# Kernel optimization log

Hardware: AMD Instinct MI355X
Metric: run time of the kernel (lower is better)

Reference implementation:

```python
import jax, jax.numpy as jnp
import numpy as np

T, K = 131072, 128  # turns, num_tags


def setup_inputs() -> dict:
    key = jax.random.key(0)
    ks = jax.random.split(key, 8)
    emissions = jax.random.normal(ks[0], (T, K), dtype=jnp.float32)
    tags = jax.random.randint(ks[1], (T,), 0, K)
    who2who = jax.random.randint(ks[2], (T - 1,), 0, 2)
    init_count = jax.random.randint(ks[3], (T - 1,), 0, 2)
    distance = jax.random.randint(ks[4], (T - 1,), 0, 3)
    class_weights = jax.random.uniform(ks[5], (K,), jnp.float32, 0.5, 1.5)
    # DistanceCRF transition matrices stacked: [s2u, u2s_n0, u2s_n1_d2, u2s_n1_dgt2]
    trans_stack = jax.random.normal(ks[6], (4, K, K), dtype=jnp.float32) * 0.1
    start_scores = jax.random.normal(ks[7], (K,), dtype=jnp.float32) * 0.1
    return {
        "emissions": emissions,
        "trans_stack": trans_stack,
        "start_scores": start_scores,
        "class_weights": class_weights,
        "tags": tags,
        "who2who": who2who,
        "init_count": init_count,
        "distance": distance,
    }


def _trans_idx(who2who, init_count, distance):
    # DistanceCRF decision tree from _get_trans:
    #   w==1 -> s2u (0); init_count==0 -> u2s_n0 (1);
    #   distance==0 -> u2s_n1_d2 (2); else -> u2s_n1_dgt2 (3)
    return jnp.where(
        who2who == 1, 0,
        jnp.where(init_count == 0, 1, jnp.where(distance == 0, 2, 3)),
    )


def reference(emissions, trans_stack, start_scores, class_weights,
              tags, who2who, init_count, distance):
    idx = _trans_idx(who2who, init_count, distance)  # [T-1]

    # ---- gold path score (fully vectorized) ----
    w = class_weights[tags]                                   # [T]
    em_gold = jnp.take_along_axis(emissions, tags[:, None], axis=1)[:, 0]  # [T]
    tr_gold = trans_stack[idx, tags[:-1], tags[1:]]           # [T-1]
    gold = w[0] * (start_scores[tags[0]] + em_gold[0]) \
        + jnp.sum(w[1:] * (tr_gold + em_gold[1:]))

    # ---- forward algorithm (log partition) ----
    def step(alphas, xs):
        i, em_t = xs
        tr = trans_stack[i]                                   # [K,K] gathered per step
        scores = alphas[:, None] + tr + em_t[None, :]         # [K,K]
        return jax.nn.logsumexp(scores, axis=0), None

    alpha0 = start_scores + emissions[0]
    alphas, _ = jax.lax.scan(step, alpha0, (idx, emissions[1:]))
    log_Z = jax.nn.logsumexp(alphas)
    return gold, log_Z
```

## Files before the change

### kernel.cpp

```cpp
#include <hip/hip_runtime.h>

#define T_LEN 131072
#define KDIM 128
#define CHUNK 16
#define WARM 16
#define NSTEP (CHUNK + WARM)
#define NCHUNK (T_LEN / CHUNK)
#define GROUPC 16
#define NGRP (NCHUNK / GROUPC)
#define CSHIFT 4.5f

typedef float v4f __attribute__((ext_vector_type(4)));
typedef short s8v __attribute__((ext_vector_type(8)));

__device__ __forceinline__ int trans_idx(int w2w, int ic, int dist) {
    return (w2w == 1) ? 0 : (ic == 0 ? 1 : (dist == 0 ? 2 : 3));
}
__device__ __forceinline__ unsigned short bf16rne(float x) {
    unsigned u = __float_as_uint(x);
    return (unsigned short)((u + 0x7fffu + ((u >> 16) & 1u)) >> 16);
}
__device__ __forceinline__ float bf16tof(unsigned short h) {
    return __uint_as_float(((unsigned)h) << 16);
}

__global__ void __launch_bounds__(256) scan_kernel(
    const float* __restrict__ em, const float* __restrict__ trans,
    const float* __restrict__ start, const float* __restrict__ cw,
    const int* __restrict__ tags, const int* __restrict__ w2w,
    const int* __restrict__ ic, const int* __restrict__ dist,
    double* __restrict__ goldslots, double* __restrict__ logzslots,
    unsigned* __restrict__ donecnt, float* __restrict__ out)
{
    const int tid = threadIdx.x;
    const int wv  = tid >> 6;
    const int ln  = tid & 63;
    const int lr  = ln & 15;
    const int hq  = ln >> 4;
    const int grp = blockIdx.x;

    __shared__ float SS[32][130];
    __shared__ __align__(16) unsigned short A[2][GROUPC * KDIM];
    __shared__ double bg[4];
    __shared__ double bzred[4];
    __shared__ double redd[256];
    __shared__ int islast;

    s8v Bf[4][2][4];
    const int ncol = (wv << 5) + lr;
    {
        const int sr = tid >> 3;
        const int sc = (tid & 7) << 4;
        float4 nx0, nx1, nx2, nx3;
        {
            const float* s = trans + (tid << 4);
            nx0 = *(const float4*)(s);     nx1 = *(const float4*)(s + 4);
            nx2 = *(const float4*)(s + 8); nx3 = *(const float4*)(s + 12);
        }
        #pragma unroll
        for (int p = 0; p < 16; ++p) {
            const int m = p >> 2, ks = p & 3;
            ((float2*)&SS[sr][sc])[0] = make_float2(nx0.x, nx0.y);
            ((float2*)&SS[sr][sc])[1] = make_float2(nx0.z, nx0.w);
            ((float2*)&SS[sr][sc + 4])[0] = make_float2(nx1.x, nx1.y);
            ((float2*)&SS[sr][sc + 4])[1] = make_float2(nx1.z, nx1.w);
            ((float2*)&SS[sr][sc + 8])[0] = make_float2(nx2.x, nx2.y);
            ((float2*)&SS[sr][sc + 8])[1] = make_float2(nx2.z, nx2.w);
            ((float2*)&SS[sr][sc + 12])[0] = make_float2(nx3.x, nx3.y);
            ((float2*)&SS[sr][sc + 12])[1] = make_float2(nx3.z, nx3.w);
            __syncthreads();
            if (p < 15) {
                const float* s = trans + ((p + 1) << 12) + (tid << 4);
                nx0 = *(const float4*)(s);     nx1 = *(const float4*)(s + 4);
                nx2 = *(const float4*)(s + 8); nx3 = *(const float4*)(s + 12);
            }
            s8v f0, f1;
            #pragma unroll
            for (int j = 0; j < 8; ++j) {
                f0[j] = (short)bf16rne(__expf(SS[(hq << 3) + j][ncol]));
                f1[j] = (short)bf16rne(__expf(SS[(hq << 3) + j][ncol + 16]));
            }
            Bf[m][0][ks] = f0;
            Bf[m][1][ks] = f1;
            __syncthreads();
        }
    }

    {
        float gp = 0.f;
        const int t = 1 + (grp << 8) + tid;
        if (t < T_LEN) {
            const int tg  = tags[t];
            const int tgp = tags[t - 1];
            const int mm  = trans_idx(w2w[t - 1], ic[t - 1], dist[t - 1]);
            gp = cw[tg] * (trans[((size_t)mm * KDIM + tgp) * KDIM + tg] +
                           em[(size_t)t * KDIM + tg]);
        }
        if (grp == 0 && tid == 0) {
            const int tg0 = tags[0];
            gp += cw[tg0] * (start[tg0] + em[tg0]);
        }
        float r = gp;
        #pragma unroll
        for (int off = 32; off; off >>= 1) r += __shfl_down(r, off, 64);
        if (ln == 0) bg[wv] = (double)r;
    }

    if (wv == 0) {
        const int c_row = (grp << 4) + lr;
        #pragma unroll
        for (int kk = 0; kk < 32; kk += 2) {
            const int k = (hq << 5) + kk;
            float a0, a1;
            if (c_row == 0) {
                a0 = __expf(start[k] + em[k]);
                a1 = __expf(start[k + 1] + em[k + 1]);
            } else { a0 = 1.f; a1 = 1.f; }
            const int off = (lr << 8) + ((k << 1) ^ ((lr & 7) << 4));
            *(unsigned*)((char*)A[0] + off) =
                (unsigned)bf16rne(a0) | ((unsigned)bf16rne(a1) << 16);
        }
    }
    __syncthreads();

    int t0r[4];
    #pragma unroll
    for (int r = 0; r < 4; ++r) {
        const int c_r = (grp << 4) + (hq << 2) + r;
        t0r[r] = (c_r == 0) ? 1 : (1 + c_r * CHUNK - WARM);
    }
    const int c_lr   = (grp << 4) + lr;
    const int town_l = 1 + c_lr * CHUNK;
    const int tend_l = min(town_l + CHUNK, T_LEN);
    const int t0_l   = (c_lr == 0) ? 1 : (town_l - WARM);

    int pmw, pmi, pmd;
    {
        const int ix = min(t0_l - 1, T_LEN - 2);
        pmw = w2w[ix]; pmi = ic[ix]; pmd = dist[ix];
    }
    float pem[2][4];
    #pragma unroll
    for (int r = 0; r < 4; ++r) {
        const int t = min(t0r[r], T_LEN - 1);
        pem[0][r] = em[(size_t)t * KDIM + ncol];
        pem[1][r] = em[(size_t)t * KDIM + ncol + 16];
    }

    float g = 0.f;
    float sc4[4] = {1.f, 1.f, 1.f, 1.f};

    for (int it = 0; it <= NSTEP; ++it) {
        s8v Af[4];
        #pragma unroll
        for (int ks = 0; ks < 4; ++ks) {
            const int off = (lr << 8) + (((ks << 6) + (hq << 4)) ^ ((lr & 7) << 4));
            Af[ks] = *(const s8v*)((const char*)A[it & 1] + off);
        }

        const bool trig = ((it & 7) == 0) || (grp == NGRP - 1 && it == NSTEP - 1);
        if (trig) {
            float s = 0.f;
            #pragma unroll
            for (int ks = 0; ks < 4; ++ks) {
                #pragma unroll
                for (int j = 0; j < 8; ++j)
                    s += bf16tof((unsigned short)Af[ks][j]);
            }
            s += __shfl_xor(s, 16, 64);
            s += __shfl_xor(s, 32, 64);
            const int tprev = t0_l + it - 1;
            const bool dn = ((tprev & 7) == 0) || (tprev == T_LEN - 1);
            const float scl = dn ? (1.f / s) : 1.f;
            if (it == 0) {
                if (c_lr == 0) g += __logf(s);
            } else if (dn && tprev >= town_l && tprev < tend_l) {
                g += __logf(s);
            }
            #pragma unroll
            for (int r = 0; r < 4; ++r) sc4[r] = __shfl(scl, (hq << 2) + r, 64);
        }
        if (it == NSTEP) break;

        const int mcur = trans_idx(pmw, pmi, pmd);
        int m4[4];
        #pragma unroll
        for (int r = 0; r < 4; ++r) m4[r] = __shfl(mcur, (hq << 2) + r, 64);
        float dv[2][4];
        #pragma unroll
        for (int nt = 0; nt < 2; ++nt) {
            #pragma unroll
            for (int r = 0; r < 4; ++r)
                dv[nt][r] = __expf(pem[nt][r] - CSHIFT) * sc4[r];
        }

        {
            const int ix = min(t0_l + it, T_LEN - 2);
            pmw = w2w[ix]; pmi = ic[ix]; pmd = dist[ix];
        }
        #pragma unroll
        for (int r = 0; r < 4; ++r) {
            const int t = min(t0r[r] + it + 1, T_LEN - 1);
            pem[0][r] = em[(size_t)t * KDIM + ncol];
            pem[1][r] = em[(size_t)t * KDIM + ncol + 16];
        }

        v4f acc[4][2];
        #pragma unroll
        for (int m = 0; m < 4; ++m) {
            #pragma unroll
            for (int nt = 0; nt < 2; ++nt) acc[m][nt] = (v4f)0.f;
        }
        #pragma unroll
        for (int ks = 0; ks < 4; ++ks) {
            #pragma unroll
            for (int m = 0; m < 4; ++m) {
                #pragma unroll
                for (int nt = 0; nt < 2; ++nt)
                    acc[m][nt] = __builtin_amdgcn_mfma_f32_16x16x32_bf16(
                        Af[ks], Bf[m][nt][ks], acc[m][nt], 0, 0, 0);
            }
        }

        #pragma unroll
        for (int nt = 0; nt < 2; ++nt) {
            #pragma unroll
            for (int r = 0; r < 4; ++r) {
                const int mm = m4[r];
                float y = acc[0][nt][r];
                y = (mm == 1) ? acc[1][nt][r] : y;
                y = (mm == 2) ? acc[2][nt][r] : y;
                y = (mm == 3) ? acc[3][nt][r] : y;
                y *= dv[nt][r];
                const int row = (hq << 2) + r;
                const int col = (wv << 5) + (nt << 4) + lr;
                const int off = (row << 8) + ((col << 1) ^ ((row & 7) << 4));
                *(unsigned short*)((char*)A[(it & 1) ^ 1] + off) = bf16rne(y);
            }
        }
        #pragma unroll
        for (int r = 0; r < 4; ++r) sc4[r] = 1.f;
        __syncthreads();
    }

    {
        float gz = (ln < 16) ? (g + CSHIFT * (float)(tend_l - town_l)) : 0.f;
        float r = gz;
        #pragma unroll
        for (int off = 32; off; off >>= 1) r += __shfl_down(r, off, 64);
        if (ln == 0) bzred[wv] = (double)r;
    }
    __syncthreads();

    if (tid == 0) {
        goldslots[grp] = bg[0] + bg[1] + bg[2] + bg[3];
        logzslots[grp] = bzred[0];
        __threadfence();
        const unsigned prev = atomicAdd(donecnt, 1u);
        islast = (prev == NGRP - 1) ? 1 : 0;
    }
    __syncthreads();
    if (islast) {
        __threadfence();
        double G = 0.0, Z = 0.0;
        #pragma unroll
        for (int k = 0; k < NGRP / 256; ++k) {
            G += goldslots[tid + (k << 8)];
            Z += logzslots[tid + (k << 8)];
        }
        redd[tid] = G;
        __syncthreads();
        for (int s = 128; s > 0; s >>= 1) {
            if (tid < s) redd[tid] += redd[tid + s];
            __syncthreads();
        }
        if (tid == 0) out[0] = (float)redd[0];
        __syncthreads();
        redd[tid] = Z;
        __syncthreads();
        for (int s = 128; s > 0; s >>= 1) {
            if (tid < s) redd[tid] += redd[tid + s];
            __syncthreads();
        }
        if (tid == 0) out[1] = (float)redd[0];
    }
}

extern "C" void kernel_launch(void* const* d_in, const int* in_sizes, int n_in,
                              void* d_out, int out_size, void* d_ws, size_t ws_size,
                              hipStream_t stream) {
    const float* emissions = (const float*)d_in[0];
    const float* trans     = (const float*)d_in[1];
    const float* start     = (const float*)d_in[2];
    const float* cw        = (const float*)d_in[3];
    const int*   tags      = (const int*)d_in[4];
    const int*   w2w       = (const int*)d_in[5];
    const int*   icnt      = (const int*)d_in[6];
    const int*   dist      = (const int*)d_in[7];

    double*   goldslots = (double*)d_ws;
    double*   logzslots = (double*)d_ws + NGRP;
    unsigned* donecnt   = (unsigned*)((double*)d_ws + 2 * NGRP);

    hipMemsetAsync(donecnt, 0, sizeof(unsigned), stream);
    scan_kernel<<<NGRP, 256, 0, stream>>>(emissions, trans, start, cw, tags,
                                          w2w, icnt, dist, goldslots, logzslots,
                                          donecnt, (float*)d_out);
}
```

Baseline: 188.7 us.

## Pack two chunk-groups per 512-thread block to share transition-matrix preprocessing

Each block now runs two independent 16-chunk groups, one per set of four waves, and launches half as many blocks with 512 threads. The exp/bf16 conversion of the transition matrices into MFMA B fragments is split across twice as many threads, so each block's setup is cheaper and is paid half as often. In exchange, the per-step __syncthreads now spans 8 waves and couples the two groups, register pressure under launch_bounds(512) may limit occupancy, and the final reduction and slot layout are reworked to match.

```diff
diff --git a/kernel.cpp b/kernel.cpp
--- a/kernel.cpp
+++ b/kernel.cpp
@@ -7,7 +7,9 @@
 #define NSTEP (CHUNK + WARM)
 #define NCHUNK (T_LEN / CHUNK)
 #define GROUPC 16
-#define NGRP (NCHUNK / GROUPC)
+#define CLUST 2
+#define NBLK (NCHUNK / (GROUPC * CLUST))
+#define NGRP2 (NCHUNK / GROUPC)
 #define CSHIFT 4.5f
 
 typedef float v4f __attribute__((ext_vector_type(4)));
@@ -24,7 +26,7 @@
     return __uint_as_float(((unsigned)h) << 16);
 }
 
-__global__ void __launch_bounds__(256) scan_kernel(
+__global__ void __launch_bounds__(512) scan_kernel(
     const float* __restrict__ em, const float* __restrict__ trans,
     const float* __restrict__ start, const float* __restrict__ cw,
     const int* __restrict__ tags, const int* __restrict__ w2w,
@@ -34,28 +36,29 @@
 {
     const int tid = threadIdx.x;
     const int wv  = tid >> 6;
+    const int cl  = wv >> 2;
+    const int wvc = wv & 3;
     const int ln  = tid & 63;
     const int lr  = ln & 15;
     const int hq  = ln >> 4;
-    const int grp = blockIdx.x;
+    const int grp2 = (blockIdx.x << 1) | cl;
 
     __shared__ float SS[32][130];
-    __shared__ __align__(16) unsigned short A[2][GROUPC * KDIM];
-    __shared__ double bg[4];
-    __shared__ double bzred[4];
+    __shared__ __align__(16) unsigned short A[CLUST][2][GROUPC * KDIM];
+    __shared__ double bg[8];
+    __shared__ double bzred[CLUST];
     __shared__ double redd[256];
     __shared__ int islast;
 
     s8v Bf[4][2][4];
-    const int ncol = (wv << 5) + lr;
+    const int ncol = (wvc << 5) + lr;
     {
-        const int sr = tid >> 3;
-        const int sc = (tid & 7) << 4;
-        float4 nx0, nx1, nx2, nx3;
+        const int sr = tid >> 4;
+        const int sc = (tid & 15) << 3;
+        float4 nx0, nx1;
         {
-            const float* s = trans + (tid << 4);
-            nx0 = *(const float4*)(s);     nx1 = *(const float4*)(s + 4);
-            nx2 = *(const float4*)(s + 8); nx3 = *(const float4*)(s + 12);
+            const float* s = trans + (tid << 3);
+            nx0 = *(const float4*)(s); nx1 = *(const float4*)(s + 4);
         }
         #pragma unroll
         for (int p = 0; p < 16; ++p) {
@@ -64,15 +67,10 @@
             ((float2*)&SS[sr][sc])[1] = make_float2(nx0.z, nx0.w);
             ((float2*)&SS[sr][sc + 4])[0] = make_float2(nx1.x, nx1.y);
             ((float2*)&SS[sr][sc + 4])[1] = make_float2(nx1.z, nx1.w);
-            ((float2*)&SS[sr][sc + 8])[0] = make_float2(nx2.x, nx2.y);
-            ((float2*)&SS[sr][sc + 8])[1] = make_float2(nx2.z, nx2.w);
-            ((float2*)&SS[sr][sc + 12])[0] = make_float2(nx3.x, nx3.y);
-            ((float2*)&SS[sr][sc + 12])[1] = make_float2(nx3.z, nx3.w);
             __syncthreads();
             if (p < 15) {
-                const float* s = trans + ((p + 1) << 12) + (tid << 4);
-                nx0 = *(const float4*)(s);     nx1 = *(const float4*)(s + 4);
-                nx2 = *(const float4*)(s + 8); nx3 = *(const float4*)(s + 12);
+                const float* s = trans + ((p + 1) << 12) + (tid << 3);
+                nx0 = *(const float4*)(s); nx1 = *(const float4*)(s + 4);
             }
             s8v f0, f1;
             #pragma unroll
@@ -88,7 +86,7 @@
 
     {
         float gp = 0.f;
-        const int t = 1 + (grp << 8) + tid;
+        const int t = 1 + (blockIdx.x << 9) + tid;
         if (t < T_LEN) {
             const int tg  = tags[t];
             const int tgp = tags[t - 1];
@@ -96,7 +94,7 @@
             gp = cw[tg] * (trans[((size_t)mm * KDIM + tgp) * KDIM + tg] +
                            em[(size_t)t * KDIM + tg]);
         }
-        if (grp == 0 && tid == 0) {
+        if (blockIdx.x == 0 && tid == 0) {
             const int tg0 = tags[0];
             gp += cw[tg0] * (start[tg0] + em[tg0]);
         }
@@ -106,8 +104,8 @@
         if (ln == 0) bg[wv] = (double)r;
     }
 
-    if (wv == 0) {
-        const int c_row = (grp << 4) + lr;
+    if (wvc == 0) {
+        const int c_row = (grp2 << 4) + lr;
         #pragma unroll
         for (int kk = 0; kk < 32; kk += 2) {
             const int k = (hq << 5) + kk;
@@ -117,7 +115,7 @@
                 a1 = __expf(start[k + 1] + em[k + 1]);
             } else { a0 = 1.f; a1 = 1.f; }
             const int off = (lr << 8) + ((k << 1) ^ ((lr & 7) << 4));
-            *(unsigned*)((char*)A[0] + off) =
+            *(unsigned*)((char*)A[cl][0] + off) =
                 (unsigned)bf16rne(a0) | ((unsigned)bf16rne(a1) << 16);
         }
     }
@@ -126,10 +124,10 @@
     int t0r[4];
     #pragma unroll
     for (int r = 0; r < 4; ++r) {
-        const int c_r = (grp << 4) + (hq << 2) + r;
+        const int c_r = (grp2 << 4) + (hq << 2) + r;
         t0r[r] = (c_r == 0) ? 1 : (1 + c_r * CHUNK - WARM);
     }
-    const int c_lr   = (grp << 4) + lr;
+    const int c_lr   = (grp2 << 4) + lr;
     const int town_l = 1 + c_lr * CHUNK;
     const int tend_l = min(town_l + CHUNK, T_LEN);
     const int t0_l   = (c_lr == 0) ? 1 : (town_l - WARM);
@@ -155,10 +153,10 @@
         #pragma unroll
         for (int ks = 0; ks < 4; ++ks) {
             const int off = (lr << 8) + (((ks << 6) + (hq << 4)) ^ ((lr & 7) << 4));
-            Af[ks] = *(const s8v*)((const char*)A[it & 1] + off);
-        }
-
-        const bool trig = ((it & 7) == 0) || (grp == NGRP - 1 && it == NSTEP - 1);
+            Af[ks] = *(const s8v*)((const char*)A[cl][it & 1] + off);
+        }
+
+        const bool trig = ((it & 7) == 0) || (grp2 == NGRP2 - 1 && it == NSTEP - 1);
         if (trig) {
             float s = 0.f;
             #pragma unroll
@@ -233,9 +231,9 @@
                 y = (mm == 3) ? acc[3][nt][r] : y;
                 y *= dv[nt][r];
                 const int row = (hq << 2) + r;
-                const int col = (wv << 5) + (nt << 4) + lr;
+                const int col = (wvc << 5) + (nt << 4) + lr;
                 const int off = (row << 8) + ((col << 1) ^ ((row & 7) << 4));
-                *(unsigned short*)((char*)A[(it & 1) ^ 1] + off) = bf16rne(y);
+                *(unsigned short*)((char*)A[cl][(it & 1) ^ 1] + off) = bf16rne(y);
             }
         }
         #pragma unroll
@@ -243,32 +241,28 @@
         __syncthreads();
     }
 
-    {
+    if (wvc == 0) {
         float gz = (ln < 16) ? (g + CSHIFT * (float)(tend_l - town_l)) : 0.f;
         float r = gz;
         #pragma unroll
         for (int off = 32; off; off >>= 1) r += __shfl_down(r, off, 64);
-        if (ln == 0) bzred[wv] = (double)r;
+        if (ln == 0) bzred[cl] = (double)r;
     }
     __syncthreads();
 
     if (tid == 0) {
-        goldslots[grp] = bg[0] + bg[1] + bg[2] + bg[3];
-        logzslots[grp] = bzred[0];
+        goldslots[blockIdx.x] = bg[0] + bg[1] + bg[2] + bg[3] +
+                                bg[4] + bg[5] + bg[6] + bg[7];
+        logzslots[(blockIdx.x << 1) | 0] = bzred[0];
+        logzslots[(blockIdx.x << 1) | 1] = bzred[1];
         __threadfence();
         const unsigned prev = atomicAdd(donecnt, 1u);
-        islast = (prev == NGRP - 1) ? 1 : 0;
+        islast = (prev == NBLK - 1) ? 1 : 0;
     }
     __syncthreads();
     if (islast) {
         __threadfence();
-        double G = 0.0, Z = 0.0;
-        #pragma unroll
-        for (int k = 0; k < NGRP / 256; ++k) {
-            G += goldslots[tid + (k << 8)];
-            Z += logzslots[tid + (k << 8)];
-        }
-        redd[tid] = G;
+        if (tid < 256) redd[tid] = goldslots[tid];
         __syncthreads();
         for (int s = 128; s > 0; s >>= 1) {
             if (tid < s) redd[tid] += redd[tid + s];
@@ -276,7 +270,7 @@
         }
         if (tid == 0) out[0] = (float)redd[0];
         __syncthreads();
-        redd[tid] = Z;
+        if (tid < 256) redd[tid] = logzslots[tid] + logzslots[tid + 256];
         __syncthreads();
         for (int s = 128; s > 0; s >>= 1) {
             if (tid < s) redd[tid] += redd[tid + s];
@@ -299,11 +293,11 @@
     const int*   dist      = (const int*)d_in[7];
 
     double*   goldslots = (double*)d_ws;
-    double*   logzslots = (double*)d_ws + NGRP;
-    unsigned* donecnt   = (unsigned*)((double*)d_ws + 2 * NGRP);
+    double*   logzslots = (double*)d_ws + 512;
+    unsigned* donecnt   = (unsigned*)((double*)d_ws + 1024);
 
     hipMemsetAsync(donecnt, 0, sizeof(unsigned), stream);
-    scan_kernel<<<NGRP, 256, 0, stream>>>(emissions, trans, start, cw, tags,
+    scan_kernel<<<NBLK, 512, 0, stream>>>(emissions, trans, start, cw, tags,
                                           w2w, icnt, dist, goldslots, logzslots,
                                           donecnt, (float*)d_out);
 }
```

New measurement: 204.8 us. 8.6% more time.
